# Performance work log

Hardware: AMD Instinct MI355X
Metric: run time of the kernel (lower is better)

## Reference

```python
import jax, jax.numpy as jnp
import numpy as np

N, F_IN = 100000, 602      # nodes, input features
H, C = 41, 1               # heads = num_classes, channels per head (hidden // heads)
E = 1600000                # raw edges (self-loops added in forward, as GATConv does)
L = 5                      # num_layers
NEG_SLOPE = 0.2


def setup_inputs() -> dict:
    key = jax.random.key(0)
    ks = jax.random.split(key, 8)
    x = jax.random.normal(ks[0], (N, F_IN), dtype=jnp.float32)
    edge_index = jax.random.randint(ks[1], (2, E), 0, N, dtype=jnp.int32)
    s = 0.1  # weight scale
    W0 = jax.random.normal(ks[2], (F_IN, H * C), dtype=jnp.float32) * s
    W_rest = jax.random.normal(ks[3], (L - 1, H * C, H * C), dtype=jnp.float32) * s
    att_src = jax.random.normal(ks[4], (L, H, C), dtype=jnp.float32) * s
    att_dst = jax.random.normal(ks[5], (L, H, C), dtype=jnp.float32) * s
    bias = jax.random.normal(ks[6], (L, H * C), dtype=jnp.float32) * s
    return {"x": x, "edge_index": edge_index, "W0": W0, "W_rest": W_rest,
            "att_src": att_src, "att_dst": att_dst, "bias": bias}


def _gat_layer(x, src, dst, W, a_s, a_d, b, apply_relu):
    n = x.shape[0]
    h = (x @ W).reshape(n, H, C)                      # per-head features [N,H,C]
    a_src_n = (h * a_s).sum(-1)                       # [N,H]
    a_dst_n = (h * a_d).sum(-1)                       # [N,H]
    e = a_src_n[src] + a_dst_n[dst]                   # [Etot,H]
    e = jnp.where(e > 0, e, NEG_SLOPE * e)            # leaky_relu
    # segment softmax over incoming edges of each dst node (self-loops => nonempty)
    emax = jax.ops.segment_max(e, dst, num_segments=n)
    ex = jnp.exp(e - emax[dst])
    denom = jax.ops.segment_sum(ex, dst, num_segments=n)
    alpha = ex / denom[dst]                           # [Etot,H]
    m = alpha[:, :, None] * h[src]                    # messages [Etot,H,C]
    out = jax.ops.segment_max(m, dst, num_segments=n) # aggr='max'
    out = out.reshape(n, H * C) + b
    return jax.nn.relu(out) if apply_relu else out


def reference(x, edge_index, W0, W_rest, att_src, att_dst, bias):
    loops = jnp.arange(N, dtype=edge_index.dtype)
    src = jnp.concatenate([edge_index[0], loops])     # add self-loops
    dst = jnp.concatenate([edge_index[1], loops])
    h = _gat_layer(x, src, dst, W0, att_src[0], att_dst[0], bias[0], True)
    for l in range(L - 1):
        last = (l == L - 2)
        h = _gat_layer(h, src, dst, W_rest[l], att_src[l + 1], att_dst[l + 1],
                       bias[l + 1], not last)
    return jax.nn.log_softmax(h, axis=1)
```

## Files before the change

kernel.cpp:

```cpp
#include <hip/hip_runtime.h>


#define N_NODES 100000
#define F_IN    602
#define NH      41
#define NEDGE   1600000
#define NLAYERS 5
#define LOG2E   1.44269504088896340736f

__global__ void hist_kernel(const int* __restrict__ dst, int* __restrict__ cnt, int e) {
    int i = blockIdx.x * blockDim.x + threadIdx.x;
    if (i < e) atomicAdd(&cnt[dst[i]], 1);
}

__global__ __launch_bounds__(1024) void scan_kernel(const int* __restrict__ cnt,
                                                    int* __restrict__ row_ptr, int n) {
    __shared__ int sums[1024];
    int t = threadIdx.x;
    int chunk = (n + 1023) >> 10;
    int start = t * chunk;
    int end   = min(start + chunk, n);
    int s = 0;
    for (int i = start; i < end; ++i) s += cnt[i];
    sums[t] = s;
    __syncthreads();
    for (int off = 1; off < 1024; off <<= 1) {
        int v = (t >= off) ? sums[t - off] : 0;
        __syncthreads();
        sums[t] += v;
        __syncthreads();
    }
    int run = (t == 0) ? 0 : sums[t - 1];
    for (int i = start; i < end; ++i) { row_ptr[i] = run; run += cnt[i]; }
    if (start < n && end == n) row_ptr[n] = run;
}

__global__ void scatter_kernel(const int* __restrict__ src, const int* __restrict__ dst,
                               const int* __restrict__ row_ptr, int* __restrict__ cur,
                               int* __restrict__ esrc, int e) {
    int i = blockIdx.x * blockDim.x + threadIdx.x;
    if (i < e) {
        int d = dst[i];
        int pos = row_ptr[d] + atomicAdd(&cur[d], 1);
        esrc[pos] = src[i];
    }
}

__global__ __launch_bounds__(256) void gemm0_kernel(const float* __restrict__ x,
                                                    const float* __restrict__ w,
                                                    float* __restrict__ h) {
    __shared__ float xs[32][257];
    int tid  = threadIdx.x;
    int row0 = blockIdx.x * 256;
    int row  = row0 + tid;

    float acc[NH];
#pragma unroll
    for (int c = 0; c < NH; ++c) acc[c] = 0.f;

    const int NCH = F_IN / 32;
    const int REM = F_IN - NCH * 32;

    for (int ci = 0; ci < NCH; ++ci) {
        int k0 = ci * 32;
#pragma unroll
        for (int li = 0; li < 32; ++li) {
            int g  = li * 256 + tid;
            int kk = g & 31;
            int r  = g >> 5;
            int rr = row0 + r;
            xs[kk][r] = (rr < N_NODES) ? x[rr * F_IN + k0 + kk] : 0.f;
        }
        __syncthreads();
#pragma unroll 4
        for (int kk = 0; kk < 32; ++kk) {
            float xv = xs[kk][tid];
#pragma unroll
            for (int c = 0; c < NH; ++c)
                acc[c] = fmaf(xv, w[(k0 + kk) * NH + c], acc[c]);
        }
        __syncthreads();
    }
    {
        int k0 = NCH * 32;
#pragma unroll
        for (int li = 0; li < 32; ++li) {
            int g  = li * 256 + tid;
            int kk = g & 31;
            int r  = g >> 5;
            int rr = row0 + r;
            xs[kk][r] = (kk < REM && rr < N_NODES) ? x[rr * F_IN + k0 + kk] : 0.f;
        }
        __syncthreads();
#pragma unroll 2
        for (int kk = 0; kk < REM; ++kk) {
            float xv = xs[kk][tid];
#pragma unroll
            for (int c = 0; c < NH; ++c)
                acc[c] = fmaf(xv, w[(k0 + kk) * NH + c], acc[c]);
        }
        __syncthreads();
    }

    if (row < N_NODES) {
#pragma unroll
        for (int c = 0; c < NH; ++c) h[row * NH + c] = acc[c];
    }
}

__global__ __launch_bounds__(256) void gemm_small_kernel(const float* __restrict__ in,
                                                         const float* __restrict__ w,
                                                         float* __restrict__ h) {
    int row = blockIdx.x * 256 + threadIdx.x;
    if (row >= N_NODES) return;
    float r[NH];
#pragma unroll
    for (int k = 0; k < NH; ++k) r[k] = in[row * NH + k];
    float acc[NH];
#pragma unroll
    for (int c = 0; c < NH; ++c) acc[c] = 0.f;
#pragma unroll 1
    for (int k = 0; k < NH; ++k) {
        float xv = r[k];
#pragma unroll
        for (int c = 0; c < NH; ++c)
            acc[c] = fmaf(xv, w[k * NH + c], acc[c]);
    }
#pragma unroll
    for (int c = 0; c < NH; ++c) h[row * NH + c] = acc[c];
}

__global__ __launch_bounds__(256) void gat_kernel(const float* __restrict__ h,
                                                  const int* __restrict__ row_ptr,
                                                  const int* __restrict__ esrc,
                                                  const float* __restrict__ att_s,
                                                  const float* __restrict__ att_d,
                                                  const float* __restrict__ bias,
                                                  float* __restrict__ out,
                                                  int apply_relu) {
    int idx = blockIdx.x * blockDim.x + threadIdx.x;
    if (idx >= N_NODES * NH) return;
    int n  = idx / NH;
    int hd = idx - n * NH;

    float as2 = att_s[hd] * LOG2E;
    float hn  = h[idx];
    float adt2 = hn * att_d[hd] * LOG2E;

    float t0 = fmaf(hn, as2, adt2);
    float e0 = fmaxf(t0, 0.2f * t0);
    float den = 1.0f;
    float num = hn;

    int s = row_ptr[n], t = row_ptr[n + 1];
    for (int j = s; j < t; ++j) {
        int   sr = esrc[j];
        float hs = h[__mul24(sr, NH) + hd];
        float tt = fmaf(hs, as2, adt2);
        float ee = fmaxf(tt, 0.2f * tt);
        float p  = __builtin_amdgcn_exp2f(ee - e0);
        den += p;
        num = fmaxf(num, p * hs);
    }
    float o = num / den + bias[hd];
    out[idx] = apply_relu ? fmaxf(o, 0.f) : o;
}

__global__ __launch_bounds__(256) void logsoftmax_kernel(const float* __restrict__ in,
                                                         float* __restrict__ out) {
    int n = blockIdx.x * blockDim.x + threadIdx.x;
    if (n >= N_NODES) return;
    float v[NH];
#pragma unroll
    for (int c = 0; c < NH; ++c) v[c] = in[n * NH + c];
    float m = v[0];
#pragma unroll
    for (int c = 1; c < NH; ++c) m = fmaxf(m, v[c]);
    float ssum = 0.f;
#pragma unroll
    for (int c = 0; c < NH; ++c) ssum += __expf(v[c] - m);
    float lg = m + logf(ssum);
#pragma unroll
    for (int c = 0; c < NH; ++c) out[n * NH + c] = v[c] - lg;
}

extern "C" void kernel_launch(void* const* d_in, const int* in_sizes, int n_in,
                              void* d_out, int out_size, void* d_ws, size_t ws_size,
                              hipStream_t stream) {
    const float* x   = (const float*)d_in[0];
    const int*   ei  = (const int*)  d_in[1];
    const float* W0  = (const float*)d_in[2];
    const float* Wr  = (const float*)d_in[3];
    const float* as_ = (const float*)d_in[4];
    const float* ad_ = (const float*)d_in[5];
    const float* bs  = (const float*)d_in[6];
    float* out = (float*)d_out;

    const int* src = ei;
    const int* dst = ei + NEDGE;

    char* ws = (char*)d_ws;
    size_t off = 0;
    auto alloc = [&](size_t bytes) -> void* {
        void* p = ws + off;
        off += (bytes + 255) & ~size_t(255);
        return p;
    };
    int*   cnt     = (int*)  alloc((size_t)N_NODES * 4);
    int*   row_ptr = (int*)  alloc((size_t)(N_NODES + 1) * 4);
    int*   esrc    = (int*)  alloc((size_t)NEDGE * 4);
    float* hbuf    = (float*)alloc((size_t)N_NODES * NH * 4);
    float* obuf    = (float*)alloc((size_t)N_NODES * NH * 4);

    hipMemsetAsync(cnt, 0, (size_t)N_NODES * 4, stream);
    hist_kernel<<<(NEDGE + 255) / 256, 256, 0, stream>>>(dst, cnt, NEDGE);
    scan_kernel<<<1, 1024, 0, stream>>>(cnt, row_ptr, N_NODES);
    hipMemsetAsync(cnt, 0, (size_t)N_NODES * 4, stream);
    scatter_kernel<<<(NEDGE + 255) / 256, 256, 0, stream>>>(src, dst, row_ptr, cnt, esrc, NEDGE);

    gemm0_kernel<<<(N_NODES + 255) / 256, 256, 0, stream>>>(x, W0, hbuf);

    for (int l = 0; l < NLAYERS; ++l) {
        if (l > 0)
            gemm_small_kernel<<<(N_NODES + 255) / 256, 256, 0, stream>>>(
                obuf, Wr + (size_t)(l - 1) * NH * NH, hbuf);
        gat_kernel<<<(N_NODES * NH + 255) / 256, 256, 0, stream>>>(
            hbuf, row_ptr, esrc, as_ + l * NH, ad_ + l * NH, bs + l * NH,
            obuf, (l < NLAYERS - 1) ? 1 : 0);
    }

    logsoftmax_kernel<<<(N_NODES + 255) / 256, 256, 0, stream>>>(obuf, out);
}
```

Before: 1.716 ms.

## Retile GEMMs into 64-row blocks with column-split waves and prefetch GAT gathers

Both GEMM kernels now process 64 rows per block, and each of the four wavefronts computes an 11-column slice of the output. The column base comes from readfirstlane, so weight reads from a transposed copy are wave-uniform. gemm0 double-buffers the x tile in shared memory, loading the next chunk into registers while the current one is computed, and gemm_small stages its input through LDS. The GAT edge loop software-prefetches two edges ahead, which requires padding esrc with zeroed entries. The aim is less register pressure, higher occupancy and hidden gather latency, at the cost of an extra transpose kernel and some overlapping column work (the last wave recomputes columns 30-32).

```diff
diff --git a/kernel.cpp b/kernel.cpp
--- a/kernel.cpp
+++ b/kernel.cpp
@@ -46,88 +46,124 @@
     }
 }
 
+__global__ void transpose_w_kernel(const float* __restrict__ W0, const float* __restrict__ Wr,
+                                   float* __restrict__ wT0, float* __restrict__ wTr) {
+    int i = blockIdx.x * blockDim.x + threadIdx.x;
+    if (i < F_IN * NH) {
+        int k = i / NH, c = i - k * NH;
+        wT0[c * F_IN + k] = W0[i];
+    }
+    if (i < 4 * NH * NH) {
+        int l = i / (NH * NH), rem = i - l * NH * NH;
+        int k = rem / NH, c = rem - k * NH;
+        wTr[l * NH * NH + c * NH + k] = Wr[i];
+    }
+}
+
 __global__ __launch_bounds__(256) void gemm0_kernel(const float* __restrict__ x,
-                                                    const float* __restrict__ w,
+                                                    const float* __restrict__ wT,
                                                     float* __restrict__ h) {
-    __shared__ float xs[32][257];
-    int tid  = threadIdx.x;
-    int row0 = blockIdx.x * 256;
-    int row  = row0 + tid;
-
-    float acc[NH];
-#pragma unroll
-    for (int c = 0; c < NH; ++c) acc[c] = 0.f;
-
-    const int NCH = F_IN / 32;
-    const int REM = F_IN - NCH * 32;
-
-    for (int ci = 0; ci < NCH; ++ci) {
+    __shared__ float xs[2][32][65];
+    const int tid  = threadIdx.x;
+    const int q    = tid >> 6;
+    const int r    = tid & 63;
+    const int rr   = tid >> 5;
+    const int kk   = tid & 31;
+    const int row0 = blockIdx.x * 64;
+    const int cbase = __builtin_amdgcn_readfirstlane(min(q * 11, NH - 11));
+    const float* __restrict__ wq = wT + cbase * F_IN;
+    const int NCHT = 19;
+
+    float acc[11];
+#pragma unroll
+    for (int c = 0; c < 11; ++c) acc[c] = 0.f;
+    float rg[8];
+
+    auto stage_load = [&](int ci) {
         int k0 = ci * 32;
-#pragma unroll
-        for (int li = 0; li < 32; ++li) {
-            int g  = li * 256 + tid;
-            int kk = g & 31;
-            int r  = g >> 5;
-            int rr = row0 + r;
-            xs[kk][r] = (rr < N_NODES) ? x[rr * F_IN + k0 + kk] : 0.f;
+        int kl = (ci == 18) ? 26 : 32;
+#pragma unroll
+        for (int li = 0; li < 8; ++li) {
+            int rrow = row0 + li * 8 + rr;
+            rg[li] = (kk < kl && rrow < N_NODES) ? x[rrow * F_IN + k0 + kk] : 0.f;
         }
+    };
+    auto stage_write = [&](int b) {
+#pragma unroll
+        for (int li = 0; li < 8; ++li) xs[b][kk][li * 8 + rr] = rg[li];
+    };
+
+    stage_load(0);
+    stage_write(0);
+
+    for (int ci = 0; ci < NCHT; ++ci) {
+        if (ci + 1 < NCHT) stage_load(ci + 1);
         __syncthreads();
-#pragma unroll 4
-        for (int kk = 0; kk < 32; ++kk) {
-            float xv = xs[kk][tid];
-#pragma unroll
-            for (int c = 0; c < NH; ++c)
-                acc[c] = fmaf(xv, w[(k0 + kk) * NH + c], acc[c]);
+        const int b = ci & 1, k0 = ci * 32;
+        if (ci < 18) {
+#pragma unroll
+            for (int k = 0; k < 32; ++k) {
+                float xv = xs[b][k][r];
+#pragma unroll
+                for (int c = 0; c < 11; ++c)
+                    acc[c] = fmaf(xv, wq[c * F_IN + k0 + k], acc[c]);
+            }
+        } else {
+#pragma unroll
+            for (int k = 0; k < 26; ++k) {
+                float xv = xs[b][k][r];
+#pragma unroll
+                for (int c = 0; c < 11; ++c)
+                    acc[c] = fmaf(xv, wq[c * F_IN + k0 + k], acc[c]);
+            }
         }
-        __syncthreads();
-    }
-    {
-        int k0 = NCH * 32;
-#pragma unroll
-        for (int li = 0; li < 32; ++li) {
-            int g  = li * 256 + tid;
-            int kk = g & 31;
-            int r  = g >> 5;
-            int rr = row0 + r;
-            xs[kk][r] = (kk < REM && rr < N_NODES) ? x[rr * F_IN + k0 + kk] : 0.f;
-        }
-        __syncthreads();
-#pragma unroll 2
-        for (int kk = 0; kk < REM; ++kk) {
-            float xv = xs[kk][tid];
-#pragma unroll
-            for (int c = 0; c < NH; ++c)
-                acc[c] = fmaf(xv, w[(k0 + kk) * NH + c], acc[c]);
-        }
-        __syncthreads();
-    }
-
+        if (ci + 1 < NCHT) stage_write((ci + 1) & 1);
+    }
+
+    int row = row0 + r;
     if (row < N_NODES) {
 #pragma unroll
-        for (int c = 0; c < NH; ++c) h[row * NH + c] = acc[c];
+        for (int c = 0; c < 11; ++c)
+            h[row * NH + cbase + c] = acc[c];
     }
 }
 
 __global__ __launch_bounds__(256) void gemm_small_kernel(const float* __restrict__ in,
-                                                         const float* __restrict__ w,
+                                                         const float* __restrict__ wT,
                                                          float* __restrict__ h) {
-    int row = blockIdx.x * 256 + threadIdx.x;
-    if (row >= N_NODES) return;
-    float r[NH];
-#pragma unroll
-    for (int k = 0; k < NH; ++k) r[k] = in[row * NH + k];
-    float acc[NH];
-#pragma unroll
-    for (int c = 0; c < NH; ++c) acc[c] = 0.f;
-#pragma unroll 1
+    __shared__ float xs[NH][65];
+    const int tid  = threadIdx.x;
+    const int q    = tid >> 6;
+    const int r    = tid & 63;
+    const int row0 = blockIdx.x * 64;
+    const int cbase = __builtin_amdgcn_readfirstlane(min(q * 11, NH - 11));
+    const float* __restrict__ wq = wT + cbase * NH;
+
+    const int base = row0 * NH;
+    for (int e = tid; e < 64 * NH; e += 256) {
+        int rrw = e / NH;
+        int k   = e - rrw * NH;
+        xs[k][rrw] = (row0 + rrw < N_NODES) ? in[base + e] : 0.f;
+    }
+    __syncthreads();
+
+    float acc[11];
+#pragma unroll
+    for (int c = 0; c < 11; ++c) acc[c] = 0.f;
+#pragma unroll
     for (int k = 0; k < NH; ++k) {
-        float xv = r[k];
-#pragma unroll
-        for (int c = 0; c < NH; ++c)
-            acc[c] = fmaf(xv, w[k * NH + c], acc[c]);
-    }
-#pragma unroll
-    for (int c = 0; c < NH; ++c) h[row * NH + c] = acc[c];
+        float xv = xs[k][r];
+#pragma unroll
+        for (int c = 0; c < 11; ++c)
+            acc[c] = fmaf(xv, wq[c * NH + k], acc[c]);
+    }
+
+    int row = row0 + r;
+    if (row < N_NODES) {
+#pragma unroll
+        for (int c = 0; c < 11; ++c)
+            h[row * NH + cbase + c] = acc[c];
+    }
 }
 
 __global__ __launch_bounds__(256) void gat_kernel(const float* __restrict__ h,
@@ -143,8 +179,8 @@
     int n  = idx / NH;
     int hd = idx - n * NH;
 
-    float as2 = att_s[hd] * LOG2E;
-    float hn  = h[idx];
+    float as2  = att_s[hd] * LOG2E;
+    float hn   = h[idx];
     float adt2 = hn * att_d[hd] * LOG2E;
 
     float t0 = fmaf(hn, as2, adt2);
@@ -153,14 +189,19 @@
     float num = hn;
 
     int s = row_ptr[n], t = row_ptr[n + 1];
+    int   sra = esrc[s];
+    int   srb = esrc[s + 1];
+    float hsa = h[__mul24(sra, NH) + hd];
+    float hsb = h[__mul24(srb, NH) + hd];
     for (int j = s; j < t; ++j) {
-        int   sr = esrc[j];
-        float hs = h[__mul24(sr, NH) + hd];
-        float tt = fmaf(hs, as2, adt2);
+        int   src2 = esrc[j + 2];
+        float hsc  = h[__mul24(src2, NH) + hd];
+        float tt = fmaf(hsa, as2, adt2);
         float ee = fmaxf(tt, 0.2f * tt);
         float p  = __builtin_amdgcn_exp2f(ee - e0);
         den += p;
-        num = fmaxf(num, p * hs);
+        num = fmaxf(num, p * hsa);
+        hsa = hsb; hsb = hsc;
     }
     float o = num / den + bias[hd];
     out[idx] = apply_relu ? fmaxf(o, 0.f) : o;
@@ -208,22 +249,28 @@
     };
     int*   cnt     = (int*)  alloc((size_t)N_NODES * 4);
     int*   row_ptr = (int*)  alloc((size_t)(N_NODES + 1) * 4);
-    int*   esrc    = (int*)  alloc((size_t)NEDGE * 4);
+    int*   esrc    = (int*)  alloc((size_t)(NEDGE + 4) * 4);
     float* hbuf    = (float*)alloc((size_t)N_NODES * NH * 4);
     float* obuf    = (float*)alloc((size_t)N_NODES * NH * 4);
+    float* wT0     = (float*)alloc((size_t)NH * F_IN * 4);
+    float* wTr     = (float*)alloc((size_t)4 * NH * NH * 4);
 
     hipMemsetAsync(cnt, 0, (size_t)N_NODES * 4, stream);
+    hipMemsetAsync(esrc + NEDGE, 0, 16, stream);
     hist_kernel<<<(NEDGE + 255) / 256, 256, 0, stream>>>(dst, cnt, NEDGE);
     scan_kernel<<<1, 1024, 0, stream>>>(cnt, row_ptr, N_NODES);
     hipMemsetAsync(cnt, 0, (size_t)N_NODES * 4, stream);
     scatter_kernel<<<(NEDGE + 255) / 256, 256, 0, stream>>>(src, dst, row_ptr, cnt, esrc, NEDGE);
 
-    gemm0_kernel<<<(N_NODES + 255) / 256, 256, 0, stream>>>(x, W0, hbuf);
+    transpose_w_kernel<<<(F_IN * NH + 255) / 256, 256, 0, stream>>>(W0, Wr, wT0, wTr);
+
+    const int NBLK = (N_NODES + 63) / 64;
+    gemm0_kernel<<<NBLK, 256, 0, stream>>>(x, wT0, hbuf);
 
     for (int l = 0; l < NLAYERS; ++l) {
         if (l > 0)
-            gemm_small_kernel<<<(N_NODES + 255) / 256, 256, 0, stream>>>(
-                obuf, Wr + (size_t)(l - 1) * NH * NH, hbuf);
+            gemm_small_kernel<<<NBLK, 256, 0, stream>>>(
+                obuf, wTr + (size_t)(l - 1) * NH * NH, hbuf);
         gat_kernel<<<(N_NODES * NH + 255) / 256, 256, 0, stream>>>(
             hbuf, row_ptr, esrc, as_ + l * NH, ad_ + l * NH, bs + l * NH,
             obuf, (l < NLAYERS - 1) ? 1 : 0);
```

Result: faster. 1.471 ms (-14.2%).
